# Optimization experiments

Measured on AMD Instinct MI355X. Metric: run time of the kernel, lower is better.

The kernel has to match this reference:

```python
import jax, jax.numpy as jnp
import numpy as np


def _skew(v):
    x, y, z = v[0], v[1], v[2]
    o = jnp.zeros((), v.dtype)
    return jnp.stack([
        jnp.stack([o, -z, y]),
        jnp.stack([z, o, -x]),
        jnp.stack([-y, x, o]),
    ])


def _so3_exp(rot):
    """Rodrigues formula, grad-safe near theta=0 (convert(..., 'so3_log'))."""
    th2 = jnp.sum(rot * rot)
    th = jnp.sqrt(th2 + 1e-30)
    a = jnp.where(th2 < 1e-12, 1.0 - th2 / 6.0, jnp.sin(th) / th)
    b = jnp.where(th2 < 1e-12, 0.5 - th2 / 24.0, (1.0 - jnp.cos(th)) / th2)
    K = _skew(rot)
    return jnp.eye(3, dtype=rot.dtype) + a * K + b * (K @ K)


def _pose(rot, xyz):
    R = _so3_exp(rot)  # [3,3]
    top = jnp.concatenate([R, xyz[:, None]], axis=1)  # [3,4]
    bot = jnp.array([[0.0, 0.0, 0.0, 1.0]], dtype=rot.dtype)
    return jnp.concatenate([top, bot], axis=0)  # [4,4]


def _trilinear(vol, pts):
    """Trilinear sample vol[D,H,W] at pts[...,3] (index coords), zeros outside."""
    dims_f = jnp.asarray(vol.shape, jnp.float32)
    dims_i = jnp.asarray(vol.shape, jnp.int32)
    p0f = jnp.floor(pts)
    f = pts - p0f
    inside = jnp.all((pts >= 0.0) & (pts <= dims_f - 1.0), axis=-1)
    i0 = jnp.clip(p0f.astype(jnp.int32), 0, dims_i - 2)
    i1 = i0 + 1
    fx, fy, fz = f[..., 0], f[..., 1], f[..., 2]
    x0, y0, z0 = i0[..., 0], i0[..., 1], i0[..., 2]
    x1, y1, z1 = i1[..., 0], i1[..., 1], i1[..., 2]
    c000 = vol[x0, y0, z0]; c001 = vol[x0, y0, z1]
    c010 = vol[x0, y1, z0]; c011 = vol[x0, y1, z1]
    c100 = vol[x1, y0, z0]; c101 = vol[x1, y0, z1]
    c110 = vol[x1, y1, z0]; c111 = vol[x1, y1, z1]
    c00 = c000 * (1 - fz) + c001 * fz
    c01 = c010 * (1 - fz) + c011 * fz
    c10 = c100 * (1 - fz) + c101 * fz
    c11 = c110 * (1 - fz) + c111 * fz
    c0 = c00 * (1 - fy) + c01 * fy
    c1 = c10 * (1 - fy) + c11 * fy
    val = c0 * (1 - fx) + c1 * fx
    return jnp.where(inside, val, 0.0)


def setup_inputs() -> dict:
    key = jax.random.key(0)
    k_vol, k_rot, k_xyz = jax.random.split(key, 3)
    D = 256
    H = W = 256
    SDD = 1020.0   # source-to-detector distance (mm)
    F = 1000.0     # focal length (px)
    volume = jax.random.uniform(k_vol, (D, D, D), dtype=jnp.float32)
    # inverse intrinsics K^{-1}
    k_inv = jnp.array([[[1.0 / F, 0.0, -(W / 2) / F],
                        [0.0, 1.0 / F, -(H / 2) / F],
                        [0.0, 0.0, 1.0]]], dtype=jnp.float32)
    # inverse extrinsics: camera (source) at (0,0,-sdd/2) in world, identity rotation
    rt_inv = jnp.eye(4, dtype=jnp.float32)[None].at[0, 2, 3].set(-SDD / 2)
    sdd = jnp.array([SDD], dtype=jnp.float32)
    eps = 1e-8
    _rot = eps * jax.random.normal(k_rot, (1, 3), dtype=jnp.float32)
    _xyz = eps * jax.random.normal(k_xyz, (1, 3), dtype=jnp.float32)
    return {"volume": volume, "rt_inv": rt_inv, "k_inv": k_inv, "sdd": sdd,
            "_rot": _rot, "_xyz": _xyz, "height": H, "width": W, "n_steps": 200}


def reference(volume, rt_inv, k_inv, sdd, _rot, _xyz, height, width, n_steps):
    # pose @ rt_inv : camera-to-world transform for this iterate
    T = _pose(_rot[0], _xyz[0]) @ rt_inv[0]  # [4,4]
    Rw, tw = T[:3, :3], T[:3, 3]
    # detector pixel centers in homogeneous pixel coords -> camera frame at depth sdd
    u = jnp.arange(width, dtype=jnp.float32) + 0.5
    v = jnp.arange(height, dtype=jnp.float32) + 0.5
    uu, vv = jnp.meshgrid(u, v, indexing="xy")  # [H,W]
    pix = jnp.stack([uu, vv, jnp.ones_like(uu)], axis=-1)  # [H,W,3]
    cam = jnp.einsum("ij,hwj->hwi", k_inv[0], pix) * sdd[0]  # detector points, camera frame
    tgt = jnp.einsum("ij,hwj->hwi", Rw, cam) + tw  # [H,W,3] world
    src = tw  # source = camera origin in world
    ray = tgt - src[None, None, :]  # [H,W,3]
    seglen = jnp.linalg.norm(ray, axis=-1) / n_steps  # [H,W]
    alphas = (jnp.arange(n_steps, dtype=jnp.float32) + 0.5) / n_steps  # [S]
    # sample points along each ray: [H,W,S,3]
    pts = src[None, None, None, :] + alphas[None, None, :, None] * ray[:, :, None, :]
    center = (jnp.asarray(volume.shape, jnp.float32) - 1.0) / 2.0
    idx = pts + center  # world (1mm spacing, volume centered at origin) -> voxel index
    vals = _trilinear(volume, idx)  # [H,W,S]
    img = vals.sum(axis=-1) * seglen  # line integral
    return img[None, None]  # [1,1,H,W]
```

## Files before the change

### kernel.cpp

```cpp
#include <hip/hip_runtime.h>
#include <math.h>


#define BLOCK  256
#define CHUNKS 8
#define PPB    (BLOCK / CHUNKS)

__global__ __launch_bounds__(BLOCK) void drr_kernel(
    const float* __restrict__ vol,
    const float* __restrict__ rt_inv,
    const float* __restrict__ k_inv,
    const float* __restrict__ sdd_p,
    const float* __restrict__ rot_p,
    const float* __restrict__ xyz_p,
    const int*   __restrict__ width_p,
    const int*   __restrict__ nsteps_p,
    float*       __restrict__ out,
    const int npix, const int D)
{
    const int tid   = (int)threadIdx.x;
    const int slot  = tid & (PPB - 1);
    const int chunk = tid / PPB;
    const int p     = (int)blockIdx.x * PPB + slot;

    float acc    = 0.0f;
    float seglen = 0.0f;

    if (p < npix) {
        const int W = *width_p;
        const int n = *nsteps_p;
        const int h = p / W;
        const int w = p - h * W;

        const float rx = rot_p[0], ry = rot_p[1], rz = rot_p[2];
        const float th2 = rx*rx + ry*ry + rz*rz;
        const float th  = sqrtf(th2 + 1e-30f);
        const float a   = (th2 < 1e-12f) ? (1.0f - th2 * (1.0f/6.0f))  : (sinf(th) / th);
        const float b   = (th2 < 1e-12f) ? (0.5f - th2 * (1.0f/24.0f)) : ((1.0f - cosf(th)) / th2);
        float Rm[3][3];
        Rm[0][0] = 1.0f + b * (-(ry*ry + rz*rz));
        Rm[0][1] = a * (-rz) + b * (rx*ry);
        Rm[0][2] = a * ( ry) + b * (rx*rz);
        Rm[1][0] = a * ( rz) + b * (rx*ry);
        Rm[1][1] = 1.0f + b * (-(rx*rx + rz*rz));
        Rm[1][2] = a * (-rx) + b * (ry*rz);
        Rm[2][0] = a * (-ry) + b * (rx*rz);
        Rm[2][1] = a * ( rx) + b * (ry*rz);
        Rm[2][2] = 1.0f + b * (-(rx*rx + ry*ry));
        const float tv[3] = { xyz_p[0], xyz_p[1], xyz_p[2] };
        const float* M = rt_inv;
        float Rw[3][3], tw[3];
        #pragma unroll
        for (int i = 0; i < 3; ++i) {
            #pragma unroll
            for (int j = 0; j < 4; ++j) {
                float s = Rm[i][0]*M[0*4+j] + Rm[i][1]*M[1*4+j]
                        + Rm[i][2]*M[2*4+j] + tv[i]*M[3*4+j];
                if (j < 3) Rw[i][j] = s; else tw[i] = s;
            }
        }

        const float sdd = sdd_p[0];
        const float u = (float)w + 0.5f;
        const float v = (float)h + 0.5f;
        const float cx = (k_inv[0]*u + k_inv[1]*v + k_inv[2]) * sdd;
        const float cy = (k_inv[3]*u + k_inv[4]*v + k_inv[5]) * sdd;
        const float cz = (k_inv[6]*u + k_inv[7]*v + k_inv[8]) * sdd;
        const float tgx = Rw[0][0]*cx + Rw[0][1]*cy + Rw[0][2]*cz + tw[0];
        const float tgy = Rw[1][0]*cx + Rw[1][1]*cy + Rw[1][2]*cz + tw[1];
        const float tgz = Rw[2][0]*cx + Rw[2][1]*cy + Rw[2][2]*cz + tw[2];
        const float rayx = tgx - tw[0];
        const float rayy = tgy - tw[1];
        const float rayz = tgz - tw[2];
        const float fn = (float)n;
        seglen = sqrtf(rayx*rayx + rayy*rayy + rayz*rayz) / fn;

        const float c    = 0.5f * (float)(D - 1);
        const float dimf = (float)(D - 1);
        const float qx = tw[0] + c, qy = tw[1] + c, qz = tw[2] + c;

        float alo = -1e30f, ahi = 1e30f;
        bool empty = false;
        {
            const float qs[3] = { qx, qy, qz };
            const float rs[3] = { rayx, rayy, rayz };
            #pragma unroll
            for (int ax = 0; ax < 3; ++ax) {
                const float q = qs[ax], r = rs[ax];
                if (fabsf(r) < 1e-20f) {
                    if (q < 0.0f || q > dimf) empty = true;
                } else {
                    const float t0 = (0.0f - q) / r;
                    const float t1 = (dimf - q) / r;
                    alo = fmaxf(alo, fminf(t0, t1));
                    ahi = fminf(ahi, fmaxf(t0, t1));
                }
            }
        }

        if (!empty && alo <= ahi) {
            int ilo = (int)ceilf (alo * fn - 0.5f) - 1;
            int ihi = (int)floorf(ahi * fn - 0.5f) + 1;
            ilo = max(ilo, 0);
            ihi = min(ihi, n - 1);
            int start = ilo + ((chunk - ilo) % CHUNKS + CHUNKS) % CHUNKS;

            const float inv_n = 1.0f / fn;
            const int DD = D * D;
            for (int i = start; i <= ihi; i += CHUNKS) {
                const float alpha = ((float)i + 0.5f) * inv_n;
                const float px = fmaf(alpha, rayx, qx);
                const float py = fmaf(alpha, rayy, qy);
                const float pz = fmaf(alpha, rayz, qz);
                const bool inside = (px >= 0.0f) & (px <= dimf)
                                  & (py >= 0.0f) & (py <= dimf)
                                  & (pz >= 0.0f) & (pz <= dimf);
                if (!inside) continue;
                const float fxf = floorf(px), fyf = floorf(py), fzf = floorf(pz);
                const float fx = px - fxf, fy = py - fyf, fz = pz - fzf;
                int x0 = min(max((int)fxf, 0), D - 2);
                int y0 = min(max((int)fyf, 0), D - 2);
                int z0 = min(max((int)fzf, 0), D - 2);
                const float* b000 = vol + (size_t)x0 * DD + (size_t)y0 * D + z0;
                const float c000 = b000[0];
                const float c001 = b000[1];
                const float c010 = b000[D];
                const float c011 = b000[D + 1];
                const float c100 = b000[DD];
                const float c101 = b000[DD + 1];
                const float c110 = b000[DD + D];
                const float c111 = b000[DD + D + 1];
                const float c00 = c000 * (1.0f - fz) + c001 * fz;
                const float c01 = c010 * (1.0f - fz) + c011 * fz;
                const float c10 = c100 * (1.0f - fz) + c101 * fz;
                const float c11 = c110 * (1.0f - fz) + c111 * fz;
                const float c0  = c00 * (1.0f - fy) + c01 * fy;
                const float c1  = c10 * (1.0f - fy) + c11 * fy;
                acc += c0 * (1.0f - fx) + c1 * fx;
            }
        }
    }

    __shared__ float red[BLOCK];
    red[tid] = acc;
    __syncthreads();
    if (tid < PPB) {
        float s = 0.0f;
        #pragma unroll
        for (int k = 0; k < CHUNKS; ++k) s += red[tid + k * PPB];
        if (p < npix) out[p] = s * seglen;
    }
}

extern "C" void kernel_launch(void* const* d_in, const int* in_sizes, int n_in,
                              void* d_out, int out_size, void* d_ws, size_t ws_size,
                              hipStream_t stream) {
    const float* vol    = (const float*)d_in[0];
    const float* rt_inv = (const float*)d_in[1];
    const float* k_inv  = (const float*)d_in[2];
    const float* sdd    = (const float*)d_in[3];
    const float* rot    = (const float*)d_in[4];
    const float* xyz    = (const float*)d_in[5];
    const int*   width  = (const int*)d_in[7];
    const int*   nsteps = (const int*)d_in[8];
    float* out = (float*)d_out;

    const int npix = out_size;
    const int D    = (int)lround(cbrt((double)in_sizes[0]));

    const int blocks = (npix + PPB - 1) / PPB;
    drr_kernel<<<blocks, BLOCK, 0, stream>>>(
        vol, rt_inv, k_inv, sdd, rot, xyz, width, nsteps, out, npix, D);
}
```

Baseline: 22.33 us.

## Transpose volume to x-innermost fp16 copy and share per-ray setup

Each call, a new kernel transposes the fp32 volume into a half-precision workspace copy with x as the fastest axis, which halves gather bytes and changes which neighbour loads share cache lines. The ray setup (pose, ray direction, clip range) is computed once per pixel by 32 threads and shared through LDS, instead of being repeated by all 8 chunk threads. The trade-off is a full read of the 64 MB volume plus a 32 MB write on every call, and a loss of precision from fp16 samples. The old path remains as a fallback when D is not 256 or the workspace is too small.

```diff
diff --git a/kernel.cpp b/kernel.cpp
--- a/kernel.cpp
+++ b/kernel.cpp
@@ -1,10 +1,208 @@
 #include <hip/hip_runtime.h>
+#include <hip/hip_fp16.h>
 #include <math.h>
 
 
 #define BLOCK  256
+#define PPB    32
 #define CHUNKS 8
-#define PPB    (BLOCK / CHUNKS)
+
+__global__ __launch_bounds__(256) void transpose_f16_kernel(
+    const float* __restrict__ vol, __half* __restrict__ T)
+{
+    __shared__ float tile[64][65];
+    const int t  = (int)threadIdx.x;
+    const int xb = (int)blockIdx.x * 64;
+    const int zb = (int)blockIdx.y * 64;
+    const int y  = (int)blockIdx.z;
+
+    const int zq = (t & 15) * 4;
+    const int xr = t >> 4;
+    #pragma unroll
+    for (int i = 0; i < 4; ++i) {
+        const int xl = xr + 16 * i;
+        const float4 v = *reinterpret_cast<const float4*>(
+            vol + ((size_t)(xb + xl) << 16) + ((size_t)y << 8) + (zb + zq));
+        tile[xl][zq + 0] = v.x;
+        tile[xl][zq + 1] = v.y;
+        tile[xl][zq + 2] = v.z;
+        tile[xl][zq + 3] = v.w;
+    }
+    __syncthreads();
+
+    const int xq = (t & 15) * 4;
+    const int zr = t >> 4;
+    #pragma unroll
+    for (int i = 0; i < 4; ++i) {
+        const int zl = zr + 16 * i;
+        const __half2 lo = __floats2half2_rn(tile[xq + 0][zl], tile[xq + 1][zl]);
+        const __half2 hi = __floats2half2_rn(tile[xq + 2][zl], tile[xq + 3][zl]);
+        uint2 pk;
+        pk.x = *reinterpret_cast<const unsigned int*>(&lo);
+        pk.y = *reinterpret_cast<const unsigned int*>(&hi);
+        *reinterpret_cast<uint2*>(
+            T + ((size_t)(zb + zl) << 16) + ((size_t)y << 8) + (xb + xq)) = pk;
+    }
+}
+
+__global__ __launch_bounds__(BLOCK) void drr_f16_kernel(
+    const __half* __restrict__ T,
+    const float* __restrict__ rt_inv,
+    const float* __restrict__ k_inv,
+    const float* __restrict__ sdd_p,
+    const float* __restrict__ rot_p,
+    const float* __restrict__ xyz_p,
+    const int*   __restrict__ width_p,
+    const int*   __restrict__ nsteps_p,
+    float*       __restrict__ out,
+    const int npix)
+{
+    const float dimf = 255.0f;
+
+    __shared__ float s_rayx[PPB], s_rayy[PPB], s_rayz[PPB], s_seglen[PPB];
+    __shared__ int   s_ilo[PPB], s_ihi[PPB];
+    __shared__ float s_q[3];
+    __shared__ float s_red[BLOCK];
+
+    const int   tid = (int)threadIdx.x;
+    const int   n   = nsteps_p[0];
+    const float fn  = (float)n;
+
+    if (tid < PPB) {
+        const int p = (int)blockIdx.x * PPB + tid;
+
+        const float rx = rot_p[0], ry = rot_p[1], rz = rot_p[2];
+        const float th2 = rx*rx + ry*ry + rz*rz;
+        const float th  = sqrtf(th2 + 1e-30f);
+        const float a   = (th2 < 1e-12f) ? (1.0f - th2 * (1.0f/6.0f))  : (sinf(th) / th);
+        const float b   = (th2 < 1e-12f) ? (0.5f - th2 * (1.0f/24.0f)) : ((1.0f - cosf(th)) / th2);
+        float Rm[3][3];
+        Rm[0][0] = 1.0f + b * (-(ry*ry + rz*rz));
+        Rm[0][1] = a * (-rz) + b * (rx*ry);
+        Rm[0][2] = a * ( ry) + b * (rx*rz);
+        Rm[1][0] = a * ( rz) + b * (rx*ry);
+        Rm[1][1] = 1.0f + b * (-(rx*rx + rz*rz));
+        Rm[1][2] = a * (-rx) + b * (ry*rz);
+        Rm[2][0] = a * (-ry) + b * (rx*rz);
+        Rm[2][1] = a * ( rx) + b * (ry*rz);
+        Rm[2][2] = 1.0f + b * (-(rx*rx + ry*ry));
+        const float tv[3] = { xyz_p[0], xyz_p[1], xyz_p[2] };
+        const float* M = rt_inv;
+        float Rw[3][3], tw[3];
+        #pragma unroll
+        for (int i = 0; i < 3; ++i) {
+            #pragma unroll
+            for (int j = 0; j < 4; ++j) {
+                float s = Rm[i][0]*M[0*4+j] + Rm[i][1]*M[1*4+j]
+                        + Rm[i][2]*M[2*4+j] + tv[i]*M[3*4+j];
+                if (j < 3) Rw[i][j] = s; else tw[i] = s;
+            }
+        }
+        const float c = 127.5f;
+        if (tid == 0) { s_q[0] = tw[0] + c; s_q[1] = tw[1] + c; s_q[2] = tw[2] + c; }
+
+        int   ilo = 0, ihi = -1;
+        float rayx = 0.f, rayy = 0.f, rayz = 0.f, seglen = 0.f;
+        if (p < npix) {
+            const int W = *width_p;
+            const int h = p / W;
+            const int w = p - h * W;
+            const float sdd = sdd_p[0];
+            const float u = (float)w + 0.5f;
+            const float v = (float)h + 0.5f;
+            const float cx = (k_inv[0]*u + k_inv[1]*v + k_inv[2]) * sdd;
+            const float cy = (k_inv[3]*u + k_inv[4]*v + k_inv[5]) * sdd;
+            const float cz = (k_inv[6]*u + k_inv[7]*v + k_inv[8]) * sdd;
+            const float tgx = Rw[0][0]*cx + Rw[0][1]*cy + Rw[0][2]*cz + tw[0];
+            const float tgy = Rw[1][0]*cx + Rw[1][1]*cy + Rw[1][2]*cz + tw[1];
+            const float tgz = Rw[2][0]*cx + Rw[2][1]*cy + Rw[2][2]*cz + tw[2];
+            rayx = tgx - tw[0];
+            rayy = tgy - tw[1];
+            rayz = tgz - tw[2];
+            seglen = sqrtf(rayx*rayx + rayy*rayy + rayz*rayz) / fn;
+
+            const float qs[3] = { tw[0] + c, tw[1] + c, tw[2] + c };
+            const float rs[3] = { rayx, rayy, rayz };
+            float alo = -1e30f, ahi = 1e30f;
+            bool empty = false;
+            #pragma unroll
+            for (int ax = 0; ax < 3; ++ax) {
+                const float q = qs[ax], r = rs[ax];
+                if (fabsf(r) < 1e-20f) {
+                    if (q < 0.0f || q > dimf) empty = true;
+                } else {
+                    const float t0 = (0.0f - q) / r;
+                    const float t1 = (dimf - q) / r;
+                    alo = fmaxf(alo, fminf(t0, t1));
+                    ahi = fminf(ahi, fmaxf(t0, t1));
+                }
+            }
+            if (!empty && alo <= ahi) {
+                ilo = (int)ceilf (alo * fn - 0.5f) - 1;
+                ihi = (int)floorf(ahi * fn - 0.5f) + 1;
+                ilo = max(ilo, 0);
+                ihi = min(ihi, n - 1);
+            }
+        }
+        s_rayx[tid] = rayx;  s_rayy[tid] = rayy;  s_rayz[tid] = rayz;
+        s_seglen[tid] = seglen;
+        s_ilo[tid] = ilo;    s_ihi[tid] = ihi;
+    }
+    __syncthreads();
+
+    const int slot  = tid & (PPB - 1);
+    const int chunk = tid >> 5;
+
+    const float rayx = s_rayx[slot], rayy = s_rayy[slot], rayz = s_rayz[slot];
+    const float qx = s_q[0], qy = s_q[1], qz = s_q[2];
+    const int ilo = s_ilo[slot], ihi = s_ihi[slot];
+
+    float acc = 0.0f;
+    const float inv_n = 1.0f / fn;
+    const int start = ilo + (((chunk - ilo) % CHUNKS) + CHUNKS) % CHUNKS;
+
+    for (int i = start; i <= ihi; i += CHUNKS) {
+        const float alpha = ((float)i + 0.5f) * inv_n;
+        const float px = fmaf(alpha, rayx, qx);
+        const float py = fmaf(alpha, rayy, qy);
+        const float pz = fmaf(alpha, rayz, qz);
+        const bool inside = (px >= 0.0f) & (px <= dimf)
+                          & (py >= 0.0f) & (py <= dimf)
+                          & (pz >= 0.0f) & (pz <= dimf);
+        if (!inside) continue;
+        const float fxf = floorf(px), fyf = floorf(py), fzf = floorf(pz);
+        const float fx = px - fxf, fy = py - fyf, fz = pz - fzf;
+        const int x0 = min(max((int)fxf, 0), 254);
+        const int y0 = min(max((int)fyf, 0), 254);
+        const int z0 = min(max((int)fzf, 0), 254);
+        const __half* bp = T + ((z0 << 16) + (y0 << 8) + x0);
+        const float c000 = __half2float(bp[0]);
+        const float c100 = __half2float(bp[1]);
+        const float c010 = __half2float(bp[256]);
+        const float c110 = __half2float(bp[257]);
+        const float c001 = __half2float(bp[65536]);
+        const float c101 = __half2float(bp[65537]);
+        const float c011 = __half2float(bp[65792]);
+        const float c111 = __half2float(bp[65793]);
+        const float c00 = c000 * (1.0f - fz) + c001 * fz;
+        const float c01 = c010 * (1.0f - fz) + c011 * fz;
+        const float c10 = c100 * (1.0f - fz) + c101 * fz;
+        const float c11 = c110 * (1.0f - fz) + c111 * fz;
+        const float c0  = c00 * (1.0f - fy) + c01 * fy;
+        const float c1  = c10 * (1.0f - fy) + c11 * fy;
+        acc += c0 * (1.0f - fx) + c1 * fx;
+    }
+
+    s_red[tid] = acc;
+    __syncthreads();
+    if (tid < PPB) {
+        float s = 0.0f;
+        #pragma unroll
+        for (int k = 0; k < CHUNKS; ++k) s += s_red[tid + k * PPB];
+        const int p = (int)blockIdx.x * PPB + tid;
+        if (p < npix) out[p] = s * s_seglen[tid];
+    }
+}
 
 __global__ __launch_bounds__(BLOCK) void drr_kernel(
     const float* __restrict__ vol,
@@ -168,7 +366,16 @@
     const int npix = out_size;
     const int D    = (int)lround(cbrt((double)in_sizes[0]));
 
+    const size_t need = (size_t)256 * 256 * 256 * sizeof(__half);
     const int blocks = (npix + PPB - 1) / PPB;
-    drr_kernel<<<blocks, BLOCK, 0, stream>>>(
-        vol, rt_inv, k_inv, sdd, rot, xyz, width, nsteps, out, npix, D);
+    if (D == 256 && ws_size >= need) {
+        __half* T = (__half*)d_ws;
+        dim3 tgrid(4, 4, 256);
+        transpose_f16_kernel<<<tgrid, 256, 0, stream>>>(vol, T);
+        drr_f16_kernel<<<blocks, BLOCK, 0, stream>>>(
+            T, rt_inv, k_inv, sdd, rot, xyz, width, nsteps, out, npix);
+    } else {
+        drr_kernel<<<blocks, BLOCK, 0, stream>>>(
+            vol, rt_inv, k_inv, sdd, rot, xyz, width, nsteps, out, npix, D);
+    }
 }
```

Result: slower. 31.92 us (+43.0%).

## Map one thread per ray with 2D pixel tiles for the fixed 256 shape

Applied to the files above, without the earlier changes.

Adds a specialised kernel for D=256 and a 256x256 image in which each thread integrates a whole ray, and each block covers a 32x8 pixel tile. This removes the per-ray step splitting and the shared-memory reduction, and aims for better cache locality among neighbouring rays. The step loop becomes branchless with a masked accumulate. The trade-offs are an eight-fold reduction in thread count, which lowers occupancy and latency hiding, and wasted loads for out-of-volume samples. Ray setup is refactored into a shared helper.

```diff
diff --git a/kernel.cpp b/kernel.cpp
--- a/kernel.cpp
+++ b/kernel.cpp
@@ -2,9 +2,157 @@
 #include <math.h>
 
 
-#define BLOCK  256
+#define BLOCK 256
+#define TU    32
+#define TV    8
 #define CHUNKS 8
 #define PPB    (BLOCK / CHUNKS)
+
+__device__ __forceinline__ void setup_ray(
+    const float* __restrict__ rt_inv, const float* __restrict__ k_inv,
+    const float sdd, const float rx, const float ry, const float rz,
+    const float tvx, const float tvy, const float tvz,
+    const int w, const int h, const int n, const int D,
+    float& rayx, float& rayy, float& rayz, float& seglen,
+    float& qx, float& qy, float& qz, int& ilo, int& ihi)
+{
+    const float th2 = rx*rx + ry*ry + rz*rz;
+    const float th  = sqrtf(th2 + 1e-30f);
+    const float a   = (th2 < 1e-12f) ? (1.0f - th2 * (1.0f/6.0f))  : (sinf(th) / th);
+    const float b   = (th2 < 1e-12f) ? (0.5f - th2 * (1.0f/24.0f)) : ((1.0f - cosf(th)) / th2);
+    float Rm[3][3];
+    Rm[0][0] = 1.0f + b * (-(ry*ry + rz*rz));
+    Rm[0][1] = a * (-rz) + b * (rx*ry);
+    Rm[0][2] = a * ( ry) + b * (rx*rz);
+    Rm[1][0] = a * ( rz) + b * (rx*ry);
+    Rm[1][1] = 1.0f + b * (-(rx*rx + rz*rz));
+    Rm[1][2] = a * (-rx) + b * (ry*rz);
+    Rm[2][0] = a * (-ry) + b * (rx*rz);
+    Rm[2][1] = a * ( rx) + b * (ry*rz);
+    Rm[2][2] = 1.0f + b * (-(rx*rx + ry*ry));
+    const float tv[3] = { tvx, tvy, tvz };
+    const float* M = rt_inv;
+    float Rw[3][3], tw[3];
+    #pragma unroll
+    for (int i = 0; i < 3; ++i) {
+        #pragma unroll
+        for (int j = 0; j < 4; ++j) {
+            float s = Rm[i][0]*M[0*4+j] + Rm[i][1]*M[1*4+j]
+                    + Rm[i][2]*M[2*4+j] + tv[i]*M[3*4+j];
+            if (j < 3) Rw[i][j] = s; else tw[i] = s;
+        }
+    }
+    const float fn = (float)n;
+    const float u = (float)w + 0.5f;
+    const float v = (float)h + 0.5f;
+    const float cx = (k_inv[0]*u + k_inv[1]*v + k_inv[2]) * sdd;
+    const float cy = (k_inv[3]*u + k_inv[4]*v + k_inv[5]) * sdd;
+    const float cz = (k_inv[6]*u + k_inv[7]*v + k_inv[8]) * sdd;
+    const float tgx = Rw[0][0]*cx + Rw[0][1]*cy + Rw[0][2]*cz + tw[0];
+    const float tgy = Rw[1][0]*cx + Rw[1][1]*cy + Rw[1][2]*cz + tw[1];
+    const float tgz = Rw[2][0]*cx + Rw[2][1]*cy + Rw[2][2]*cz + tw[2];
+    rayx = tgx - tw[0];
+    rayy = tgy - tw[1];
+    rayz = tgz - tw[2];
+    seglen = sqrtf(rayx*rayx + rayy*rayy + rayz*rayz) / fn;
+
+    const float c    = 0.5f * (float)(D - 1);
+    const float dimf = (float)(D - 1);
+    qx = tw[0] + c; qy = tw[1] + c; qz = tw[2] + c;
+
+    float alo = -1e30f, ahi = 1e30f;
+    bool empty = false;
+    const float qs[3] = { qx, qy, qz };
+    const float rs[3] = { rayx, rayy, rayz };
+    #pragma unroll
+    for (int ax = 0; ax < 3; ++ax) {
+        const float q = qs[ax], r = rs[ax];
+        if (fabsf(r) < 1e-20f) {
+            if (q < 0.0f || q > dimf) empty = true;
+        } else {
+            const float t0 = (0.0f - q) / r;
+            const float t1 = (dimf - q) / r;
+            alo = fmaxf(alo, fminf(t0, t1));
+            ahi = fminf(ahi, fmaxf(t0, t1));
+        }
+    }
+    ilo = 0; ihi = -1;
+    if (!empty && alo <= ahi) {
+        ilo = (int)ceilf (alo * fn - 0.5f) - 1;
+        ihi = (int)floorf(ahi * fn - 0.5f) + 1;
+        ilo = max(ilo, 0);
+        ihi = min(ihi, n - 1);
+    }
+}
+
+template <int DC>
+__global__ __launch_bounds__(BLOCK) void drr_tile_kernel(
+    const float* __restrict__ vol,
+    const float* __restrict__ rt_inv,
+    const float* __restrict__ k_inv,
+    const float* __restrict__ sdd_p,
+    const float* __restrict__ rot_p,
+    const float* __restrict__ xyz_p,
+    const int*   __restrict__ nsteps_p,
+    float*       __restrict__ out,
+    const int W)
+{
+    const int   D    = DC;
+    const int   DD   = D * D;
+    const float dimf = (float)(D - 1);
+
+    const int tid = (int)threadIdx.x;
+    const int bi  = (int)blockIdx.x;
+    const int nbu = W / TU;
+    const int u0  = (bi % nbu) * TU;
+    const int v0  = (bi / nbu) * TV;
+    const int w   = u0 + (tid & (TU - 1));
+    const int h   = v0 + (tid >> 5);
+
+    const int n = nsteps_p[0];
+    float rayx, rayy, rayz, seglen, qx, qy, qz;
+    int ilo, ihi;
+    setup_ray(rt_inv, k_inv, sdd_p[0], rot_p[0], rot_p[1], rot_p[2],
+              xyz_p[0], xyz_p[1], xyz_p[2], w, h, n, D,
+              rayx, rayy, rayz, seglen, qx, qy, qz, ilo, ihi);
+
+    float acc = 0.0f;
+    const float inv_n = 1.0f / (float)n;
+
+    for (int i = ilo; i <= ihi; ++i) {
+        const float alpha = ((float)i + 0.5f) * inv_n;
+        const float px = fmaf(alpha, rayx, qx);
+        const float py = fmaf(alpha, rayy, qy);
+        const float pz = fmaf(alpha, rayz, qz);
+        const bool inside = (px >= 0.0f) & (px <= dimf)
+                          & (py >= 0.0f) & (py <= dimf)
+                          & (pz >= 0.0f) & (pz <= dimf);
+        const float fxf = floorf(px), fyf = floorf(py), fzf = floorf(pz);
+        const float fx = px - fxf, fy = py - fyf, fz = pz - fzf;
+        const int x0 = min(max((int)fxf, 0), D - 2);
+        const int y0 = min(max((int)fyf, 0), D - 2);
+        const int z0 = min(max((int)fzf, 0), D - 2);
+        const float* b000 = vol + ((size_t)x0 * DD + (size_t)y0 * D + z0);
+        const float c000 = b000[0];
+        const float c001 = b000[1];
+        const float c010 = b000[D];
+        const float c011 = b000[D + 1];
+        const float c100 = b000[DD];
+        const float c101 = b000[DD + 1];
+        const float c110 = b000[DD + D];
+        const float c111 = b000[DD + D + 1];
+        const float c00 = c000 * (1.0f - fz) + c001 * fz;
+        const float c01 = c010 * (1.0f - fz) + c011 * fz;
+        const float c10 = c100 * (1.0f - fz) + c101 * fz;
+        const float c11 = c110 * (1.0f - fz) + c111 * fz;
+        const float c0  = c00 * (1.0f - fy) + c01 * fy;
+        const float c1  = c10 * (1.0f - fy) + c11 * fy;
+        const float val = c0 * (1.0f - fx) + c1 * fx;
+        acc += inside ? val : 0.0f;
+    }
+
+    out[h * W + w] = acc * seglen;
+}
 
 __global__ __launch_bounds__(BLOCK) void drr_kernel(
     const float* __restrict__ vol,
@@ -31,80 +179,15 @@
         const int n = *nsteps_p;
         const int h = p / W;
         const int w = p - h * W;
-
-        const float rx = rot_p[0], ry = rot_p[1], rz = rot_p[2];
-        const float th2 = rx*rx + ry*ry + rz*rz;
-        const float th  = sqrtf(th2 + 1e-30f);
-        const float a   = (th2 < 1e-12f) ? (1.0f - th2 * (1.0f/6.0f))  : (sinf(th) / th);
-        const float b   = (th2 < 1e-12f) ? (0.5f - th2 * (1.0f/24.0f)) : ((1.0f - cosf(th)) / th2);
-        float Rm[3][3];
-        Rm[0][0] = 1.0f + b * (-(ry*ry + rz*rz));
-        Rm[0][1] = a * (-rz) + b * (rx*ry);
-        Rm[0][2] = a * ( ry) + b * (rx*rz);
-        Rm[1][0] = a * ( rz) + b * (rx*ry);
-        Rm[1][1] = 1.0f + b * (-(rx*rx + rz*rz));
-        Rm[1][2] = a * (-rx) + b * (ry*rz);
-        Rm[2][0] = a * (-ry) + b * (rx*rz);
-        Rm[2][1] = a * ( rx) + b * (ry*rz);
-        Rm[2][2] = 1.0f + b * (-(rx*rx + ry*ry));
-        const float tv[3] = { xyz_p[0], xyz_p[1], xyz_p[2] };
-        const float* M = rt_inv;
-        float Rw[3][3], tw[3];
-        #pragma unroll
-        for (int i = 0; i < 3; ++i) {
-            #pragma unroll
-            for (int j = 0; j < 4; ++j) {
-                float s = Rm[i][0]*M[0*4+j] + Rm[i][1]*M[1*4+j]
-                        + Rm[i][2]*M[2*4+j] + tv[i]*M[3*4+j];
-                if (j < 3) Rw[i][j] = s; else tw[i] = s;
-            }
-        }
-
-        const float sdd = sdd_p[0];
-        const float u = (float)w + 0.5f;
-        const float v = (float)h + 0.5f;
-        const float cx = (k_inv[0]*u + k_inv[1]*v + k_inv[2]) * sdd;
-        const float cy = (k_inv[3]*u + k_inv[4]*v + k_inv[5]) * sdd;
-        const float cz = (k_inv[6]*u + k_inv[7]*v + k_inv[8]) * sdd;
-        const float tgx = Rw[0][0]*cx + Rw[0][1]*cy + Rw[0][2]*cz + tw[0];
-        const float tgy = Rw[1][0]*cx + Rw[1][1]*cy + Rw[1][2]*cz + tw[1];
-        const float tgz = Rw[2][0]*cx + Rw[2][1]*cy + Rw[2][2]*cz + tw[2];
-        const float rayx = tgx - tw[0];
-        const float rayy = tgy - tw[1];
-        const float rayz = tgz - tw[2];
+        float rayx, rayy, rayz, qx, qy, qz;
+        int ilo, ihi;
+        setup_ray(rt_inv, k_inv, sdd_p[0], rot_p[0], rot_p[1], rot_p[2],
+                  xyz_p[0], xyz_p[1], xyz_p[2], w, h, n, D,
+                  rayx, rayy, rayz, seglen, qx, qy, qz, ilo, ihi);
+        const float dimf = (float)(D - 1);
         const float fn = (float)n;
-        seglen = sqrtf(rayx*rayx + rayy*rayy + rayz*rayz) / fn;
-
-        const float c    = 0.5f * (float)(D - 1);
-        const float dimf = (float)(D - 1);
-        const float qx = tw[0] + c, qy = tw[1] + c, qz = tw[2] + c;
-
-        float alo = -1e30f, ahi = 1e30f;
-        bool empty = false;
-        {
-            const float qs[3] = { qx, qy, qz };
-            const float rs[3] = { rayx, rayy, rayz };
-            #pragma unroll
-            for (int ax = 0; ax < 3; ++ax) {
-                const float q = qs[ax], r = rs[ax];
-                if (fabsf(r) < 1e-20f) {
-                    if (q < 0.0f || q > dimf) empty = true;
-                } else {
-                    const float t0 = (0.0f - q) / r;
-                    const float t1 = (dimf - q) / r;
-                    alo = fmaxf(alo, fminf(t0, t1));
-                    ahi = fminf(ahi, fmaxf(t0, t1));
-                }
-            }
-        }
-
-        if (!empty && alo <= ahi) {
-            int ilo = (int)ceilf (alo * fn - 0.5f) - 1;
-            int ihi = (int)floorf(ahi * fn - 0.5f) + 1;
-            ilo = max(ilo, 0);
-            ihi = min(ihi, n - 1);
+        if (ihi >= ilo) {
             int start = ilo + ((chunk - ilo) % CHUNKS + CHUNKS) % CHUNKS;
-
             const float inv_n = 1.0f / fn;
             const int DD = D * D;
             for (int i = start; i <= ihi; i += CHUNKS) {
@@ -167,8 +250,15 @@
 
     const int npix = out_size;
     const int D    = (int)lround(cbrt((double)in_sizes[0]));
-
-    const int blocks = (npix + PPB - 1) / PPB;
-    drr_kernel<<<blocks, BLOCK, 0, stream>>>(
-        vol, rt_inv, k_inv, sdd, rot, xyz, width, nsteps, out, npix, D);
-}
+    const int W    = 256;
+
+    if (D == 256 && npix == 65536) {
+        const int blocks = npix / BLOCK;
+        drr_tile_kernel<256><<<blocks, BLOCK, 0, stream>>>(
+            vol, rt_inv, k_inv, sdd, rot, xyz, nsteps, out, W);
+    } else {
+        const int blocks = (npix + PPB - 1) / PPB;
+        drr_kernel<<<blocks, BLOCK, 0, stream>>>(
+            vol, rt_inv, k_inv, sdd, rot, xyz, width, nsteps, out, npix, D);
+    }
+}
```

Result: no change. 22.20 us (-0.5%).

## Add cache-warming prefetch kernel over the volume region the rays touch

Applied to the files above, without the earlier changes.

Adds a separate kernel that traces the four corner rays to bound the x/y voxel range the projection will sample. It then streams that sub-volume with float4 loads so it is resident in cache before the main ray-marching kernel runs. The per-ray setup is moved into a shared helper used by both kernels. The prefetch only runs for a 256^3 volume with a 256x256 detector. It adds a second launch and a full read of the bounded region, which may be wasted if the volume is already cached across calls.

```diff
diff --git a/kernel.cpp b/kernel.cpp
--- a/kernel.cpp
+++ b/kernel.cpp
@@ -5,6 +5,156 @@
 #define BLOCK  256
 #define CHUNKS 8
 #define PPB    (BLOCK / CHUNKS)
+
+__device__ __forceinline__ void setup_ray(
+    const float* __restrict__ rt_inv, const float* __restrict__ k_inv,
+    const float sdd, const float rx, const float ry, const float rz,
+    const float tvx, const float tvy, const float tvz,
+    const int w, const int h, const int n, const int D,
+    float& rayx, float& rayy, float& rayz, float& seglen,
+    float& qx, float& qy, float& qz, int& ilo, int& ihi,
+    float& aLoF, float& aHiF)
+{
+    const float th2 = rx*rx + ry*ry + rz*rz;
+    const float th  = sqrtf(th2 + 1e-30f);
+    const float a   = (th2 < 1e-12f) ? (1.0f - th2 * (1.0f/6.0f))  : (sinf(th) / th);
+    const float b   = (th2 < 1e-12f) ? (0.5f - th2 * (1.0f/24.0f)) : ((1.0f - cosf(th)) / th2);
+    float Rm[3][3];
+    Rm[0][0] = 1.0f + b * (-(ry*ry + rz*rz));
+    Rm[0][1] = a * (-rz) + b * (rx*ry);
+    Rm[0][2] = a * ( ry) + b * (rx*rz);
+    Rm[1][0] = a * ( rz) + b * (rx*ry);
+    Rm[1][1] = 1.0f + b * (-(rx*rx + rz*rz));
+    Rm[1][2] = a * (-rx) + b * (ry*rz);
+    Rm[2][0] = a * (-ry) + b * (rx*rz);
+    Rm[2][1] = a * ( rx) + b * (ry*rz);
+    Rm[2][2] = 1.0f + b * (-(rx*rx + ry*ry));
+    const float tv[3] = { tvx, tvy, tvz };
+    const float* M = rt_inv;
+    float Rw[3][3], tw[3];
+    #pragma unroll
+    for (int i = 0; i < 3; ++i) {
+        #pragma unroll
+        for (int j = 0; j < 4; ++j) {
+            float s = Rm[i][0]*M[0*4+j] + Rm[i][1]*M[1*4+j]
+                    + Rm[i][2]*M[2*4+j] + tv[i]*M[3*4+j];
+            if (j < 3) Rw[i][j] = s; else tw[i] = s;
+        }
+    }
+    const float fn = (float)n;
+    const float u = (float)w + 0.5f;
+    const float v = (float)h + 0.5f;
+    const float cx = (k_inv[0]*u + k_inv[1]*v + k_inv[2]) * sdd;
+    const float cy = (k_inv[3]*u + k_inv[4]*v + k_inv[5]) * sdd;
+    const float cz = (k_inv[6]*u + k_inv[7]*v + k_inv[8]) * sdd;
+    const float tgx = Rw[0][0]*cx + Rw[0][1]*cy + Rw[0][2]*cz + tw[0];
+    const float tgy = Rw[1][0]*cx + Rw[1][1]*cy + Rw[1][2]*cz + tw[1];
+    const float tgz = Rw[2][0]*cx + Rw[2][1]*cy + Rw[2][2]*cz + tw[2];
+    rayx = tgx - tw[0];
+    rayy = tgy - tw[1];
+    rayz = tgz - tw[2];
+    seglen = sqrtf(rayx*rayx + rayy*rayy + rayz*rayz) / fn;
+
+    const float c    = 0.5f * (float)(D - 1);
+    const float dimf = (float)(D - 1);
+    qx = tw[0] + c; qy = tw[1] + c; qz = tw[2] + c;
+
+    float alo = -1e30f, ahi = 1e30f;
+    bool empty = false;
+    const float qs[3] = { qx, qy, qz };
+    const float rs[3] = { rayx, rayy, rayz };
+    #pragma unroll
+    for (int ax = 0; ax < 3; ++ax) {
+        const float q = qs[ax], r = rs[ax];
+        if (fabsf(r) < 1e-20f) {
+            if (q < 0.0f || q > dimf) empty = true;
+        } else {
+            const float t0 = (0.0f - q) / r;
+            const float t1 = (dimf - q) / r;
+            alo = fmaxf(alo, fminf(t0, t1));
+            ahi = fminf(ahi, fmaxf(t0, t1));
+        }
+    }
+    ilo = 0; ihi = -1;
+    aLoF = 1e30f; aHiF = -1e30f;
+    if (!empty && alo <= ahi) {
+        aLoF = alo; aHiF = ahi;
+        ilo = (int)ceilf (alo * fn - 0.5f) - 1;
+        ihi = (int)floorf(ahi * fn - 0.5f) + 1;
+        ilo = max(ilo, 0);
+        ihi = min(ihi, n - 1);
+    }
+}
+
+template <int DC>
+__global__ __launch_bounds__(256) void warm_kernel(
+    const float* __restrict__ vol,
+    const float* __restrict__ rt_inv,
+    const float* __restrict__ k_inv,
+    const float* __restrict__ sdd_p,
+    const float* __restrict__ rot_p,
+    const float* __restrict__ xyz_p,
+    const int*   __restrict__ nsteps_p,
+    const int W, const int H)
+{
+    const int D = DC;
+    const int n = nsteps_p[0];
+    const float inv_n = 1.0f / (float)n;
+
+    float rxmin = 1e30f, rxmax = -1e30f, rymin = 1e30f, rymax = -1e30f;
+    float aLoB = 1e30f, aHiB = -1e30f;
+    float qx = 0.f, qy = 0.f, qz = 0.f;
+    const int cu[4] = { 0, W - 1, 0, W - 1 };
+    const int cv[4] = { 0, 0, H - 1, H - 1 };
+    #pragma unroll
+    for (int k = 0; k < 4; ++k) {
+        float crx, cry, crz, csl, cqx, cqy, cqz, cal, cah;
+        int d1, d2;
+        setup_ray(rt_inv, k_inv, sdd_p[0], rot_p[0], rot_p[1], rot_p[2],
+                  xyz_p[0], xyz_p[1], xyz_p[2], cu[k], cv[k], n, D,
+                  crx, cry, crz, csl, cqx, cqy, cqz, d1, d2, cal, cah);
+        rxmin = fminf(rxmin, crx); rxmax = fmaxf(rxmax, crx);
+        rymin = fminf(rymin, cry); rymax = fmaxf(rymax, cry);
+        if (cal <= cah) { aLoB = fminf(aLoB, cal); aHiB = fmaxf(aHiB, cah); }
+        qx = cqx; qy = cqy; qz = cqz;
+    }
+    if (aLoB > aHiB) return;
+    aLoB = fmaxf(0.0f, aLoB - 2.0f * inv_n);
+    aHiB = fminf(1.0f, aHiB + 2.0f * inv_n);
+    const float xlo = fminf(qx + aLoB * rxmin, qx + aHiB * rxmin);
+    const float xhi = fmaxf(qx + aLoB * rxmax, qx + aHiB * rxmax);
+    const float ylo = fminf(qy + aLoB * rymin, qy + aHiB * rymin);
+    const float yhi = fmaxf(qy + aLoB * rymax, qy + aHiB * rymax);
+    const int X0 = min(max((int)floorf(xlo) - 1, 0), D - 1);
+    const int X1 = min(max((int)floorf(xhi) + 2, 0), D - 1);
+    const int Y0 = min(max((int)floorf(ylo) - 1, 0), D - 1);
+    const int Y1 = min(max((int)floorf(yhi) + 2, 0), D - 1);
+    const int ny    = Y1 - Y0 + 1;
+    const int ncol4 = (X1 - X0 + 1) * ny * (D >> 2);
+
+    const int stride = (int)gridDim.x * 256;
+    for (int f0 = (int)blockIdx.x * 256 + (int)threadIdx.x;
+         f0 < ncol4; f0 += stride * 8) {
+        float s[8];
+        #pragma unroll
+        for (int k = 0; k < 8; ++k) {
+            const int f = f0 + k * stride;
+            s[k] = 0.0f;
+            if (f < ncol4) {
+                const int col = f >> 6;
+                const int zi  = (f & 63) << 2;
+                const int cx  = col / ny;
+                const int cy  = col - cx * ny;
+                const float4 v = *(const float4*)(
+                    vol + (((size_t)(X0 + cx)) << 16)
+                        + ((size_t)(Y0 + cy) << 8) + zi);
+                s[k] = v.x + v.y + v.z + v.w;
+            }
+        }
+        asm volatile("" :: "v"(s[0]), "v"(s[1]), "v"(s[2]), "v"(s[3]),
+                           "v"(s[4]), "v"(s[5]), "v"(s[6]), "v"(s[7]));
+    }
+}
 
 __global__ __launch_bounds__(BLOCK) void drr_kernel(
     const float* __restrict__ vol,
@@ -31,80 +181,15 @@
         const int n = *nsteps_p;
         const int h = p / W;
         const int w = p - h * W;
-
-        const float rx = rot_p[0], ry = rot_p[1], rz = rot_p[2];
-        const float th2 = rx*rx + ry*ry + rz*rz;
-        const float th  = sqrtf(th2 + 1e-30f);
-        const float a   = (th2 < 1e-12f) ? (1.0f - th2 * (1.0f/6.0f))  : (sinf(th) / th);
-        const float b   = (th2 < 1e-12f) ? (0.5f - th2 * (1.0f/24.0f)) : ((1.0f - cosf(th)) / th2);
-        float Rm[3][3];
-        Rm[0][0] = 1.0f + b * (-(ry*ry + rz*rz));
-        Rm[0][1] = a * (-rz) + b * (rx*ry);
-        Rm[0][2] = a * ( ry) + b * (rx*rz);
-        Rm[1][0] = a * ( rz) + b * (rx*ry);
-        Rm[1][1] = 1.0f + b * (-(rx*rx + rz*rz));
-        Rm[1][2] = a * (-rx) + b * (ry*rz);
-        Rm[2][0] = a * (-ry) + b * (rx*rz);
-        Rm[2][1] = a * ( rx) + b * (ry*rz);
-        Rm[2][2] = 1.0f + b * (-(rx*rx + ry*ry));
-        const float tv[3] = { xyz_p[0], xyz_p[1], xyz_p[2] };
-        const float* M = rt_inv;
-        float Rw[3][3], tw[3];
-        #pragma unroll
-        for (int i = 0; i < 3; ++i) {
-            #pragma unroll
-            for (int j = 0; j < 4; ++j) {
-                float s = Rm[i][0]*M[0*4+j] + Rm[i][1]*M[1*4+j]
-                        + Rm[i][2]*M[2*4+j] + tv[i]*M[3*4+j];
-                if (j < 3) Rw[i][j] = s; else tw[i] = s;
-            }
-        }
-
-        const float sdd = sdd_p[0];
-        const float u = (float)w + 0.5f;
-        const float v = (float)h + 0.5f;
-        const float cx = (k_inv[0]*u + k_inv[1]*v + k_inv[2]) * sdd;
-        const float cy = (k_inv[3]*u + k_inv[4]*v + k_inv[5]) * sdd;
-        const float cz = (k_inv[6]*u + k_inv[7]*v + k_inv[8]) * sdd;
-        const float tgx = Rw[0][0]*cx + Rw[0][1]*cy + Rw[0][2]*cz + tw[0];
-        const float tgy = Rw[1][0]*cx + Rw[1][1]*cy + Rw[1][2]*cz + tw[1];
-        const float tgz = Rw[2][0]*cx + Rw[2][1]*cy + Rw[2][2]*cz + tw[2];
-        const float rayx = tgx - tw[0];
-        const float rayy = tgy - tw[1];
-        const float rayz = tgz - tw[2];
+        float rayx, rayy, rayz, qx, qy, qz, dal, dah;
+        int ilo, ihi;
+        setup_ray(rt_inv, k_inv, sdd_p[0], rot_p[0], rot_p[1], rot_p[2],
+                  xyz_p[0], xyz_p[1], xyz_p[2], w, h, n, D,
+                  rayx, rayy, rayz, seglen, qx, qy, qz, ilo, ihi, dal, dah);
+        const float dimf = (float)(D - 1);
         const float fn = (float)n;
-        seglen = sqrtf(rayx*rayx + rayy*rayy + rayz*rayz) / fn;
-
-        const float c    = 0.5f * (float)(D - 1);
-        const float dimf = (float)(D - 1);
-        const float qx = tw[0] + c, qy = tw[1] + c, qz = tw[2] + c;
-
-        float alo = -1e30f, ahi = 1e30f;
-        bool empty = false;
-        {
-            const float qs[3] = { qx, qy, qz };
-            const float rs[3] = { rayx, rayy, rayz };
-            #pragma unroll
-            for (int ax = 0; ax < 3; ++ax) {
-                const float q = qs[ax], r = rs[ax];
-                if (fabsf(r) < 1e-20f) {
-                    if (q < 0.0f || q > dimf) empty = true;
-                } else {
-                    const float t0 = (0.0f - q) / r;
-                    const float t1 = (dimf - q) / r;
-                    alo = fmaxf(alo, fminf(t0, t1));
-                    ahi = fminf(ahi, fmaxf(t0, t1));
-                }
-            }
-        }
-
-        if (!empty && alo <= ahi) {
-            int ilo = (int)ceilf (alo * fn - 0.5f) - 1;
-            int ihi = (int)floorf(ahi * fn - 0.5f) + 1;
-            ilo = max(ilo, 0);
-            ihi = min(ihi, n - 1);
+        if (ihi >= ilo) {
             int start = ilo + ((chunk - ilo) % CHUNKS + CHUNKS) % CHUNKS;
-
             const float inv_n = 1.0f / fn;
             const int DD = D * D;
             for (int i = start; i <= ihi; i += CHUNKS) {
@@ -168,6 +253,10 @@
     const int npix = out_size;
     const int D    = (int)lround(cbrt((double)in_sizes[0]));
 
+    if (D == 256 && npix == 65536) {
+        warm_kernel<256><<<1024, 256, 0, stream>>>(
+            vol, rt_inv, k_inv, sdd, rot, xyz, nsteps, 256, 256);
+    }
     const int blocks = (npix + PPB - 1) / PPB;
     drr_kernel<<<blocks, BLOCK, 0, stream>>>(
         vol, rt_inv, k_inv, sdd, rot, xyz, width, nsteps, out, npix, D);
```

Measured after the change: 36.43 us. +63.2%, slower.
